# Optimization experiments

Measured on AMD Instinct MI355X. Metric: run time of the kernel, lower is better.

The kernel has to match this reference:

```python
import jax, jax.numpy as jnp
import numpy as np

B, H, P, L = 8, 512, 512, 2048
HIGH_STAB, LOW_STAB = 0.9, 0.99  # 0 <= high < |lambda| <= low <= 1 (discrete dynamics)


def setup_inputs() -> dict:
    key = jax.random.key(0)
    k_u, k_mag, k_ph, k_b, k_c, k_d = jax.random.split(key, 6)
    u = jax.random.normal(k_u, (B, H, L), dtype=jnp.float32)
    # Frozen diagonal reservoir state matrix Lambda_bar: complex eigenvalues with
    # magnitude in (high_stability, low_stability], random phase (stored as real/imag pairs).
    mag = jax.random.uniform(k_mag, (P,), minval=HIGH_STAB, maxval=LOW_STAB)
    phase = jax.random.uniform(k_ph, (P,), minval=0.0, maxval=2.0 * np.pi)
    Lambda_bar_ri = jnp.stack([mag * jnp.cos(phase), mag * jnp.sin(phase)], axis=-1)  # (P,2)
    B_bar_ri = jax.random.normal(k_b, (P, H, 2), dtype=jnp.float32)  # complex B_bar as real pairs
    C_ri = jax.random.normal(k_c, (H, P, 2), dtype=jnp.float32)      # complex C as real pairs
    D = jax.random.normal(k_d, (H, H), dtype=jnp.float32)
    return {"u": u, "Lambda_bar_ri": Lambda_bar_ri, "B_bar_ri": B_bar_ri, "C_ri": C_ri, "D": D}


def _binary_op(e_i, e_j):
    A_i, Bu_i = e_i
    A_j, Bu_j = e_j
    return (A_j * A_i, A_j * Bu_i + Bu_j)


def reference(u, Lambda_bar_ri, B_bar_ri, C_ri, D):
    Lam = jax.lax.complex(Lambda_bar_ri[:, 0], Lambda_bar_ri[:, 1])        # (P,)
    B_bar = jax.lax.complex(B_bar_ri[..., 0], B_bar_ri[..., 1])            # (P,H)
    C = jax.lax.complex(C_ri[..., 0], C_ri[..., 1])                        # (H,P)
    # Bu_t = B_bar @ u_t for all t, batched: (B,P,L) complex
    Bu = jnp.einsum('ph,bhl->bpl', B_bar, u.astype(B_bar.dtype))
    A = jnp.broadcast_to(Lam[None, :, None], Bu.shape)                     # (B,P,L)
    # Parallel associative scan: x_t = Lam * x_{t-1} + Bu_t
    _, x = jax.lax.associative_scan(_binary_op, (A, Bu), axis=2)           # (B,P,L)
    C_A_Bu = jnp.einsum('hp,bpl->bhl', C, x).real                          # (B,H,L)
    # torch.einsum('hh,bhl->bhl', D, u) uses only the diagonal of D
    Du = jnp.diagonal(D)[None, :, None] * u
    return jax.nn.gelu(C_A_Bu + Du, approximate=False)
```

## Files before the change

kernel.cpp:

```cpp
#include <hip/hip_runtime.h>
#include <cstdint>
#include <cstddef>

#define BB 8
#define HH 512
#define PP 512
#define LL 2048

typedef __attribute__((ext_vector_type(8))) __bf16 bf16x8;
typedef __attribute__((ext_vector_type(4))) float f32x4;

__device__ __forceinline__ uint16_t f2bf(float f) {
  uint32_t u = __builtin_bit_cast(uint32_t, f);
  u += 0x7FFFu + ((u >> 16) & 1u);
  return (uint16_t)(u >> 16);
}

__global__ __launch_bounds__(256) void prep_mats(
    const float* __restrict__ Bbar, const float* __restrict__ Cri,
    const float* __restrict__ Dm,
    uint16_t* __restrict__ A1, uint16_t* __restrict__ A2,
    float* __restrict__ Dd) {
  int idx = blockIdx.x * 256 + threadIdx.x;
  int p = idx >> 9, h = idx & 511;
  A1[(size_t)p * 512 + h]          = f2bf(Bbar[((size_t)p * 512 + h) * 2 + 0]);
  A1[(size_t)(512 + p) * 512 + h]  = f2bf(Bbar[((size_t)p * 512 + h) * 2 + 1]);
  int h2 = idx >> 9, p2 = idx & 511;
  A2[(size_t)h2 * 1024 + p2]        = f2bf( Cri[((size_t)h2 * 512 + p2) * 2 + 0]);
  A2[(size_t)h2 * 1024 + 512 + p2]  = f2bf(-Cri[((size_t)h2 * 512 + p2) * 2 + 1]);
  if (idx < 512) Dd[idx] = Dm[(size_t)idx * 512 + idx];
}

__global__ __launch_bounds__(256) void scan_kernel(
    const float* __restrict__ Lam, uint16_t* __restrict__ Bu) {
  const int gt = blockIdx.x * 256 + threadIdx.x;
  const int wave = gt >> 6, lane = gt & 63;
  const int b = wave >> 9, p = wave & 511;
  const float lr = Lam[p * 2 + 0], li = Lam[p * 2 + 1];
  float ar = lr, ai = li;
#pragma unroll
  for (int s = 0; s < 5; ++s) { float nr = ar * ar - ai * ai, ni = 2.f * ar * ai; ar = nr; ai = ni; }

  uint16_t* rowre = Bu + ((size_t)(b * 1024 + p)) * 2048 + lane * 32;
  uint16_t* rowim = Bu + ((size_t)(b * 1024 + 512 + p)) * 2048 + lane * 32;
  uint4 vr[4], vi[4];
#pragma unroll
  for (int q = 0; q < 4; ++q) { vr[q] = ((const uint4*)rowre)[q]; vi[q] = ((const uint4*)rowim)[q]; }

  float xr[32], xi[32];
  float sr = 0.f, si = 0.f;
#pragma unroll
  for (int q = 0; q < 4; ++q) {
    uint32_t wr[4] = {vr[q].x, vr[q].y, vr[q].z, vr[q].w};
    uint32_t wi[4] = {vi[q].x, vi[q].y, vi[q].z, vi[q].w};
#pragma unroll
    for (int d = 0; d < 4; ++d) {
      float br0 = __builtin_bit_cast(float, wr[d] << 16);
      float bi0 = __builtin_bit_cast(float, wi[d] << 16);
      float br1 = __builtin_bit_cast(float, wr[d] & 0xFFFF0000u);
      float bi1 = __builtin_bit_cast(float, wi[d] & 0xFFFF0000u);
      int j = q * 8 + d * 2;
      float nr = lr * sr - li * si + br0, ni = lr * si + li * sr + bi0;
      sr = nr; si = ni; xr[j] = sr; xi[j] = si;
      nr = lr * sr - li * si + br1; ni = lr * si + li * sr + bi1;
      sr = nr; si = ni; xr[j + 1] = sr; xi[j + 1] = si;
    }
  }
  float Ar = ar, Ai = ai, Sr = sr, Si = si;
#pragma unroll
  for (int off = 1; off < 64; off <<= 1) {
    float pAr = __shfl_up(Ar, off), pAi = __shfl_up(Ai, off);
    float pSr = __shfl_up(Sr, off), pSi = __shfl_up(Si, off);
    if (lane >= off) {
      float tSr = Ar * pSr - Ai * pSi + Sr;
      float tSi = Ar * pSi + Ai * pSr + Si;
      float tAr = Ar * pAr - Ai * pAi;
      float tAi = Ar * pAi + Ai * pAr;
      Sr = tSr; Si = tSi; Ar = tAr; Ai = tAi;
    }
  }
  float Cr = __shfl_up(Sr, 1), Ci = __shfl_up(Si, 1);
  if (lane == 0) { Cr = 0.f; Ci = 0.f; }
  float fr_ = lr * Cr - li * Ci, fi_ = lr * Ci + li * Cr;
#pragma unroll
  for (int j = 0; j < 32; ++j) {
    xr[j] += fr_; xi[j] += fi_;
    float nfr = fr_ * lr - fi_ * li, nfi = fr_ * li + fi_ * lr;
    fr_ = nfr; fi_ = nfi;
  }
#pragma unroll
  for (int q = 0; q < 4; ++q) {
    uint32_t wr[4], wi[4];
#pragma unroll
    for (int d = 0; d < 4; ++d) {
      int j = q * 8 + d * 2;
      wr[d] = (uint32_t)f2bf(xr[j]) | ((uint32_t)f2bf(xr[j + 1]) << 16);
      wi[d] = (uint32_t)f2bf(xi[j]) | ((uint32_t)f2bf(xi[j + 1]) << 16);
    }
    ((uint4*)rowre)[q] = make_uint4(wr[0], wr[1], wr[2], wr[3]);
    ((uint4*)rowim)[q] = make_uint4(wi[0], wi[1], wi[2], wi[3]);
  }
}

__global__ __launch_bounds__(512) void gemm1_fused(
    const uint16_t* __restrict__ A, const float* __restrict__ U,
    uint16_t* __restrict__ Bu) {
  __shared__ __align__(16) uint16_t Blds[2][64 * 136];
  const int t = threadIdx.x, lane = t & 63, w = t >> 6;
  const int m0 = blockIdx.y * 512, n0 = blockIdx.x * 64, b = blockIdx.z;
  const int fr = lane & 15, fq = lane >> 4;

  const int kr = t >> 3, lc = t & 7;
  const int wcol = (((kr >> 2) ^ lc) << 3) + (kr & 3) * 2;
  const float* gB = U + ((size_t)b * 512 + 2 * kr) * 2048 + n0 + lc * 8;

  const uint16_t* gA = A + (size_t)(m0 + w * 64 + fr) * 512 + fq * 8;

  f32x4 acc[4][4];
#pragma unroll
  for (int i = 0; i < 4; ++i)
#pragma unroll
    for (int j = 0; j < 4; ++j) acc[i][j] = (f32x4){0.f, 0.f, 0.f, 0.f};

  int rb[4], hj[4];
#pragma unroll
  for (int j = 0; j < 4; ++j) { int n = j * 16 + fr; rb[j] = n * 136; hj[j] = n >> 3; }

  float4 p0, p1, p2, p3;
  p0 = *(const float4*)(gB);
  p1 = *(const float4*)(gB + 4);
  p2 = *(const float4*)(gB + 2048);
  p3 = *(const float4*)(gB + 2052);
  {
    float r0[8] = {p0.x, p0.y, p0.z, p0.w, p1.x, p1.y, p1.z, p1.w};
    float r1[8] = {p2.x, p2.y, p2.z, p2.w, p3.x, p3.y, p3.z, p3.w};
#pragma unroll
    for (int j = 0; j < 8; ++j)
      *(uint32_t*)&Blds[0][(lc * 8 + j) * 136 + wcol] =
          (uint32_t)f2bf(r0[j]) | ((uint32_t)f2bf(r1[j]) << 16);
  }
  bf16x8 afr[2][4];
#pragma unroll
  for (int i = 0; i < 4; ++i) afr[0][i] = *(const bf16x8*)(gA + i * 8192);
  __syncthreads();

  for (int p = 0; p < 4; ++p) {
    const int cb = p & 1;
    if (p < 3) {
      const float* sp = gB + (size_t)((p + 1) * 128) * 2048;
      p0 = *(const float4*)(sp);
      p1 = *(const float4*)(sp + 4);
      p2 = *(const float4*)(sp + 2048);
      p3 = *(const float4*)(sp + 2052);
    }
#pragma unroll
    for (int s = 0; s < 4; ++s) {
      if (p < 3 || s < 3) {
        const int ks = p * 128 + (s + 1) * 32;
#pragma unroll
        for (int i = 0; i < 4; ++i)
          afr[(s + 1) & 1][i] = *(const bf16x8*)(gA + i * 8192 + ks);
      }
      bf16x8 bfr[4];
#pragma unroll
      for (int j = 0; j < 4; ++j)
        bfr[j] = *(const bf16x8*)&Blds[cb][rb[j] + ((((s * 4 + fq) ^ hj[j])) << 3)];
#pragma unroll
      for (int i = 0; i < 4; ++i)
#pragma unroll
        for (int j = 0; j < 4; ++j)
          acc[i][j] = __builtin_amdgcn_mfma_f32_16x16x32_bf16(afr[s & 1][i], bfr[j], acc[i][j], 0, 0, 0);
    }
    if (p < 3) {
      float r0[8] = {p0.x, p0.y, p0.z, p0.w, p1.x, p1.y, p1.z, p1.w};
      float r1[8] = {p2.x, p2.y, p2.z, p2.w, p3.x, p3.y, p3.z, p3.w};
#pragma unroll
      for (int j = 0; j < 8; ++j)
        *(uint32_t*)&Blds[cb ^ 1][(lc * 8 + j) * 136 + wcol] =
            (uint32_t)f2bf(r0[j]) | ((uint32_t)f2bf(r1[j]) << 16);
      __syncthreads();
    }
  }

  uint16_t* O = Bu + ((size_t)b * 1024 + m0 + w * 64) * 2048 + n0;
#pragma unroll
  for (int i = 0; i < 4; ++i)
#pragma unroll
    for (int j = 0; j < 4; ++j)
#pragma unroll
      for (int r = 0; r < 4; ++r)
        O[(size_t)(i * 16 + fq * 4 + r) * 2048 + j * 16 + fr] = f2bf(acc[i][j][r]);
}

__global__ __launch_bounds__(512) void gemm2_fused(
    const uint16_t* __restrict__ A, const uint16_t* __restrict__ X,
    float* __restrict__ Out, const float* __restrict__ Dd,
    const float* __restrict__ Uu) {
  __shared__ __align__(16) uint16_t Blds[2][64 * 136];
  const int t = threadIdx.x, lane = t & 63, w = t >> 6;
  const int n0 = blockIdx.x * 64, b = blockIdx.z;
  const int fr = lane & 15, fq = lane >> 4;

  const int kr = t >> 3, lc = t & 7;
  const int wcol = (((kr >> 2) ^ lc) << 3) + (kr & 3) * 2;
  const uint16_t* gB = X + ((size_t)b * 1024 + 2 * kr) * 2048 + n0 + lc * 8;

  const uint16_t* gA = A + (size_t)(w * 64 + fr) * 1024 + fq * 8;

  f32x4 acc[4][4];
#pragma unroll
  for (int i = 0; i < 4; ++i)
#pragma unroll
    for (int j = 0; j < 4; ++j) acc[i][j] = (f32x4){0.f, 0.f, 0.f, 0.f};

  int rb[4], hj[4];
#pragma unroll
  for (int j = 0; j < 4; ++j) { int n = j * 16 + fr; rb[j] = n * 136; hj[j] = n >> 3; }

  uint4 q0, q1;
  q0 = *(const uint4*)(gB);
  q1 = *(const uint4*)(gB + 2048);
  {
    uint32_t u0[4] = {q0.x, q0.y, q0.z, q0.w};
    uint32_t u1[4] = {q1.x, q1.y, q1.z, q1.w};
#pragma unroll
    for (int d = 0; d < 4; ++d) {
      *(uint32_t*)&Blds[0][(lc * 8 + 2 * d + 0) * 136 + wcol] = (u0[d] & 0xFFFFu) | (u1[d] << 16);
      *(uint32_t*)&Blds[0][(lc * 8 + 2 * d + 1) * 136 + wcol] = (u0[d] >> 16) | (u1[d] & 0xFFFF0000u);
    }
  }
  bf16x8 afr[2][4];
#pragma unroll
  for (int i = 0; i < 4; ++i) afr[0][i] = *(const bf16x8*)(gA + i * 16384);
  __syncthreads();

  for (int p = 0; p < 8; ++p) {
    const int cb = p & 1;
    if (p < 7) {
      const uint16_t* sp = gB + (size_t)((p + 1) * 128) * 2048;
      q0 = *(const uint4*)(sp);
      q1 = *(const uint4*)(sp + 2048);
    }
#pragma unroll
    for (int s = 0; s < 4; ++s) {
      if (p < 7 || s < 3) {
        const int ks = p * 128 + (s + 1) * 32;
#pragma unroll
        for (int i = 0; i < 4; ++i)
          afr[(s + 1) & 1][i] = *(const bf16x8*)(gA + i * 16384 + ks);
      }
      bf16x8 bfr[4];
#pragma unroll
      for (int j = 0; j < 4; ++j)
        bfr[j] = *(const bf16x8*)&Blds[cb][rb[j] + ((((s * 4 + fq) ^ hj[j])) << 3)];
#pragma unroll
      for (int i = 0; i < 4; ++i)
#pragma unroll
        for (int j = 0; j < 4; ++j)
          acc[i][j] = __builtin_amdgcn_mfma_f32_16x16x32_bf16(afr[s & 1][i], bfr[j], acc[i][j], 0, 0, 0);
    }
    if (p < 7) {
      uint32_t u0[4] = {q0.x, q0.y, q0.z, q0.w};
      uint32_t u1[4] = {q1.x, q1.y, q1.z, q1.w};
#pragma unroll
      for (int d = 0; d < 4; ++d) {
        *(uint32_t*)&Blds[cb ^ 1][(lc * 8 + 2 * d + 0) * 136 + wcol] = (u0[d] & 0xFFFFu) | (u1[d] << 16);
        *(uint32_t*)&Blds[cb ^ 1][(lc * 8 + 2 * d + 1) * 136 + wcol] = (u0[d] >> 16) | (u1[d] & 0xFFFF0000u);
      }
      __syncthreads();
    }
  }

  const size_t base = ((size_t)b * 512 + w * 64) * 2048 + n0;
  float* O = Out + base;
  const float* Ub = Uu + base;
#pragma unroll
  for (int i = 0; i < 4; ++i)
#pragma unroll
    for (int r = 0; r < 4; ++r) {
      int mm = i * 16 + fq * 4 + r;
      float dv = Dd[w * 64 + mm];
#pragma unroll
      for (int j = 0; j < 4; ++j) {
        int nn = j * 16 + fr;
        float xv = acc[i][j][r] + dv * Ub[(size_t)mm * 2048 + nn];
        O[(size_t)mm * 2048 + nn] = 0.5f * xv * (1.f + erff(xv * 0.70710678118654752f));
      }
    }
}

extern "C" void kernel_launch(void* const* d_in, const int* in_sizes, int n_in,
                              void* d_out, int out_size, void* d_ws, size_t ws_size,
                              hipStream_t stream) {
  const float* u    = (const float*)d_in[0];
  const float* Lam  = (const float*)d_in[1];
  const float* Bbar = (const float*)d_in[2];
  const float* Cri  = (const float*)d_in[3];
  const float* Dm   = (const float*)d_in[4];
  float* out = (float*)d_out;

  char* ws = (char*)d_ws;
  uint16_t* Bu = (uint16_t*)(ws);
  uint16_t* A1 = (uint16_t*)(ws + 33554432);
  uint16_t* A2 = (uint16_t*)(ws + 34603008);
  float*    Dd = (float*)   (ws + 35651584);

  prep_mats<<<1024, 256, 0, stream>>>(Bbar, Cri, Dm, A1, A2, Dd);
  gemm1_fused<<<dim3(32, 2, BB), 512, 0, stream>>>(A1, u, Bu);
  scan_kernel<<<1024, 256, 0, stream>>>(Lam, Bu);
  gemm2_fused<<<dim3(32, 1, BB), 512, 0, stream>>>(A2, Bu, out, Dd, u);
}
```

Measured before the change: 205.3 us.

## Coalesce scan loads/stores via LDS transpose and split gemm2 M across blocks

The scan kernel now stages each wave's row through swizzled shared memory. Global loads and stores become fully coalesced 16-byte accesses instead of each lane touching a strided 64-byte chunk. gemm2 drops to 256 threads with 4 waves, and each block covers half of M (256 rows), which doubles the grid to 512 blocks for better CU occupancy. Each thread in gemm2 now loads two B rows per stage to fill the same LDS tile, so more redundant B traffic crosses the two M halves.

```diff
diff --git a/kernel.cpp b/kernel.cpp
--- a/kernel.cpp
+++ b/kernel.cpp
@@ -33,19 +33,32 @@
 
 __global__ __launch_bounds__(256) void scan_kernel(
     const float* __restrict__ Lam, uint16_t* __restrict__ Bu) {
-  const int gt = blockIdx.x * 256 + threadIdx.x;
-  const int wave = gt >> 6, lane = gt & 63;
+  __shared__ uint4 lds[4][2][256];
+  const int t = threadIdx.x, lane = t & 63, wv = t >> 6;
+  const int wave = blockIdx.x * 4 + wv;
   const int b = wave >> 9, p = wave & 511;
   const float lr = Lam[p * 2 + 0], li = Lam[p * 2 + 1];
   float ar = lr, ai = li;
 #pragma unroll
   for (int s = 0; s < 5; ++s) { float nr = ar * ar - ai * ai, ni = 2.f * ar * ai; ar = nr; ai = ni; }
 
-  uint16_t* rowre = Bu + ((size_t)(b * 1024 + p)) * 2048 + lane * 32;
-  uint16_t* rowim = Bu + ((size_t)(b * 1024 + 512 + p)) * 2048 + lane * 32;
+  uint4* gre = (uint4*)(Bu + ((size_t)(b * 1024 + p)) * 2048);
+  uint4* gim = (uint4*)(Bu + ((size_t)(b * 1024 + 512 + p)) * 2048);
+
+#pragma unroll
+  for (int q = 0; q < 4; ++q) {
+    int c = 64 * q + lane, s = c ^ ((c >> 2) & 7);
+    lds[wv][0][s] = gre[c];
+    lds[wv][1][s] = gim[c];
+  }
+  __builtin_amdgcn_wave_barrier();
   uint4 vr[4], vi[4];
 #pragma unroll
-  for (int q = 0; q < 4; ++q) { vr[q] = ((const uint4*)rowre)[q]; vi[q] = ((const uint4*)rowim)[q]; }
+  for (int d = 0; d < 4; ++d) {
+    int c = 4 * lane + d, s = c ^ (lane & 7);
+    vr[d] = lds[wv][0][s];
+    vi[d] = lds[wv][1][s];
+  }
 
   float xr[32], xi[32];
   float sr = 0.f, si = 0.f;
@@ -97,8 +110,16 @@
       wr[d] = (uint32_t)f2bf(xr[j]) | ((uint32_t)f2bf(xr[j + 1]) << 16);
       wi[d] = (uint32_t)f2bf(xi[j]) | ((uint32_t)f2bf(xi[j + 1]) << 16);
     }
-    ((uint4*)rowre)[q] = make_uint4(wr[0], wr[1], wr[2], wr[3]);
-    ((uint4*)rowim)[q] = make_uint4(wi[0], wi[1], wi[2], wi[3]);
+    int c = 4 * lane + q, s = c ^ (lane & 7);
+    lds[wv][0][s] = make_uint4(wr[0], wr[1], wr[2], wr[3]);
+    lds[wv][1][s] = make_uint4(wi[0], wi[1], wi[2], wi[3]);
+  }
+  __builtin_amdgcn_wave_barrier();
+#pragma unroll
+  for (int q = 0; q < 4; ++q) {
+    int c = 64 * q + lane, s = c ^ ((c >> 2) & 7);
+    gre[c] = lds[wv][0][s];
+    gim[c] = lds[wv][1][s];
   }
 }
 
@@ -192,20 +213,22 @@
         O[(size_t)(i * 16 + fq * 4 + r) * 2048 + j * 16 + fr] = f2bf(acc[i][j][r]);
 }
 
-__global__ __launch_bounds__(512) void gemm2_fused(
+__global__ __launch_bounds__(256) void gemm2_fused(
     const uint16_t* __restrict__ A, const uint16_t* __restrict__ X,
     float* __restrict__ Out, const float* __restrict__ Dd,
     const float* __restrict__ Uu) {
   __shared__ __align__(16) uint16_t Blds[2][64 * 136];
   const int t = threadIdx.x, lane = t & 63, w = t >> 6;
-  const int n0 = blockIdx.x * 64, b = blockIdx.z;
+  const int m0 = blockIdx.y * 256, n0 = blockIdx.x * 64, b = blockIdx.z;
   const int fr = lane & 15, fq = lane >> 4;
 
   const int kr = t >> 3, lc = t & 7;
-  const int wcol = (((kr >> 2) ^ lc) << 3) + (kr & 3) * 2;
-  const uint16_t* gB = X + ((size_t)b * 1024 + 2 * kr) * 2048 + n0 + lc * 8;
-
-  const uint16_t* gA = A + (size_t)(w * 64 + fr) * 1024 + fq * 8;
+  const int wcolA = (((kr >> 2) ^ lc) << 3) + (kr & 3) * 2;
+  const int wcolB = ((((kr >> 2) + 8) ^ lc) << 3) + (kr & 3) * 2;
+  const uint16_t* gBa = X + ((size_t)b * 1024 + 2 * kr) * 2048 + n0 + lc * 8;
+  const uint16_t* gBb = gBa + (size_t)64 * 2048;
+
+  const uint16_t* gA = A + (size_t)(m0 + w * 64 + fr) * 1024 + fq * 8;
 
   f32x4 acc[4][4];
 #pragma unroll
@@ -217,16 +240,22 @@
 #pragma unroll
   for (int j = 0; j < 4; ++j) { int n = j * 16 + fr; rb[j] = n * 136; hj[j] = n >> 3; }
 
-  uint4 q0, q1;
-  q0 = *(const uint4*)(gB);
-  q1 = *(const uint4*)(gB + 2048);
+  uint4 qa0, qa1, qb0, qb1;
+  qa0 = *(const uint4*)(gBa);
+  qa1 = *(const uint4*)(gBa + 2048);
+  qb0 = *(const uint4*)(gBb);
+  qb1 = *(const uint4*)(gBb + 2048);
   {
-    uint32_t u0[4] = {q0.x, q0.y, q0.z, q0.w};
-    uint32_t u1[4] = {q1.x, q1.y, q1.z, q1.w};
+    uint32_t u0[4] = {qa0.x, qa0.y, qa0.z, qa0.w};
+    uint32_t u1[4] = {qa1.x, qa1.y, qa1.z, qa1.w};
+    uint32_t v0[4] = {qb0.x, qb0.y, qb0.z, qb0.w};
+    uint32_t v1[4] = {qb1.x, qb1.y, qb1.z, qb1.w};
 #pragma unroll
     for (int d = 0; d < 4; ++d) {
-      *(uint32_t*)&Blds[0][(lc * 8 + 2 * d + 0) * 136 + wcol] = (u0[d] & 0xFFFFu) | (u1[d] << 16);
-      *(uint32_t*)&Blds[0][(lc * 8 + 2 * d + 1) * 136 + wcol] = (u0[d] >> 16) | (u1[d] & 0xFFFF0000u);
+      *(uint32_t*)&Blds[0][(lc * 8 + 2 * d + 0) * 136 + wcolA] = (u0[d] & 0xFFFFu) | (u1[d] << 16);
+      *(uint32_t*)&Blds[0][(lc * 8 + 2 * d + 1) * 136 + wcolA] = (u0[d] >> 16) | (u1[d] & 0xFFFF0000u);
+      *(uint32_t*)&Blds[0][(lc * 8 + 2 * d + 0) * 136 + wcolB] = (v0[d] & 0xFFFFu) | (v1[d] << 16);
+      *(uint32_t*)&Blds[0][(lc * 8 + 2 * d + 1) * 136 + wcolB] = (v0[d] >> 16) | (v1[d] & 0xFFFF0000u);
     }
   }
   bf16x8 afr[2][4];
@@ -237,9 +266,11 @@
   for (int p = 0; p < 8; ++p) {
     const int cb = p & 1;
     if (p < 7) {
-      const uint16_t* sp = gB + (size_t)((p + 1) * 128) * 2048;
-      q0 = *(const uint4*)(sp);
-      q1 = *(const uint4*)(sp + 2048);
+      const uint16_t* spa = gBa + (size_t)((p + 1) * 128) * 2048;
+      qa0 = *(const uint4*)(spa);
+      qa1 = *(const uint4*)(spa + 2048);
+      qb0 = *(const uint4*)(spa + (size_t)64 * 2048);
+      qb1 = *(const uint4*)(spa + (size_t)65 * 2048);
     }
 #pragma unroll
     for (int s = 0; s < 4; ++s) {
@@ -260,18 +291,22 @@
           acc[i][j] = __builtin_amdgcn_mfma_f32_16x16x32_bf16(afr[s & 1][i], bfr[j], acc[i][j], 0, 0, 0);
     }
     if (p < 7) {
-      uint32_t u0[4] = {q0.x, q0.y, q0.z, q0.w};
-      uint32_t u1[4] = {q1.x, q1.y, q1.z, q1.w};
+      uint32_t u0[4] = {qa0.x, qa0.y, qa0.z, qa0.w};
+      uint32_t u1[4] = {qa1.x, qa1.y, qa1.z, qa1.w};
+      uint32_t v0[4] = {qb0.x, qb0.y, qb0.z, qb0.w};
+      uint32_t v1[4] = {qb1.x, qb1.y, qb1.z, qb1.w};
 #pragma unroll
       for (int d = 0; d < 4; ++d) {
-        *(uint32_t*)&Blds[cb ^ 1][(lc * 8 + 2 * d + 0) * 136 + wcol] = (u0[d] & 0xFFFFu) | (u1[d] << 16);
-        *(uint32_t*)&Blds[cb ^ 1][(lc * 8 + 2 * d + 1) * 136 + wcol] = (u0[d] >> 16) | (u1[d] & 0xFFFF0000u);
+        *(uint32_t*)&Blds[cb ^ 1][(lc * 8 + 2 * d + 0) * 136 + wcolA] = (u0[d] & 0xFFFFu) | (u1[d] << 16);
+        *(uint32_t*)&Blds[cb ^ 1][(lc * 8 + 2 * d + 1) * 136 + wcolA] = (u0[d] >> 16) | (u1[d] & 0xFFFF0000u);
+        *(uint32_t*)&Blds[cb ^ 1][(lc * 8 + 2 * d + 0) * 136 + wcolB] = (v0[d] & 0xFFFFu) | (v1[d] << 16);
+        *(uint32_t*)&Blds[cb ^ 1][(lc * 8 + 2 * d + 1) * 136 + wcolB] = (v0[d] >> 16) | (v1[d] & 0xFFFF0000u);
       }
       __syncthreads();
     }
   }
 
-  const size_t base = ((size_t)b * 512 + w * 64) * 2048 + n0;
+  const size_t base = ((size_t)b * 512 + m0 + w * 64) * 2048 + n0;
   float* O = Out + base;
   const float* Ub = Uu + base;
 #pragma unroll
@@ -279,7 +314,7 @@
 #pragma unroll
     for (int r = 0; r < 4; ++r) {
       int mm = i * 16 + fq * 4 + r;
-      float dv = Dd[w * 64 + mm];
+      float dv = Dd[m0 + w * 64 + mm];
 #pragma unroll
       for (int j = 0; j < 4; ++j) {
         int nn = j * 16 + fr;
@@ -308,5 +343,5 @@
   prep_mats<<<1024, 256, 0, stream>>>(Bbar, Cri, Dm, A1, A2, Dd);
   gemm1_fused<<<dim3(32, 2, BB), 512, 0, stream>>>(A1, u, Bu);
   scan_kernel<<<1024, 256, 0, stream>>>(Lam, Bu);
-  gemm2_fused<<<dim3(32, 1, BB), 512, 0, stream>>>(A2, Bu, out, Dd, u);
-}
+  gemm2_fused<<<dim3(32, 2, BB), 256, 0, stream>>>(A2, Bu, out, Dd, u);
+}
```

New measurement: 195.6 us. 4.7% less time.
